# Performance work log

Hardware: AMD Instinct MI355X
Metric: run time of the kernel (lower is better)

## Reference

```python
import jax, jax.numpy as jnp
import numpy as np

LN_EPS = 1e-5

def _layernorm(x, g, b):
    mu = jnp.mean(x, axis=-1, keepdims=True)
    var = jnp.mean(jnp.square(x - mu), axis=-1, keepdims=True)
    return (x - mu) * jax.lax.rsqrt(var + LN_EPS) * g + b

def setup_inputs() -> dict:
    key = jax.random.key(0)
    ks = jax.random.split(key, 12)
    N0, N1, D0, D1, DO, E = 50000, 50000, 256, 512, 256, 1600000
    return {
        "x0": jax.random.normal(ks[0], (N0, D0), jnp.float32),
        "x1": jax.random.normal(ks[1], (N1, D1), jnp.float32),
        "W0": jax.random.normal(ks[2], (D0, DO), jnp.float32) * 0.05,
        "W1": jax.random.normal(ks[3], (D1, DO), jnp.float32) * 0.05,
        "Wres1": jax.random.normal(ks[4], (D1, DO), jnp.float32) * 0.05,
        "g0": jnp.ones((DO,), jnp.float32),
        "b0": jnp.zeros((DO,), jnp.float32),
        "g1": jnp.ones((DO,), jnp.float32),
        "b1": jnp.zeros((DO,), jnp.float32),
        "ew0": jax.random.uniform(ks[5], (E,), jnp.float32),
        "ew1": jax.random.uniform(ks[6], (E,), jnp.float32),
        "row0": jax.random.randint(ks[7], (E,), 0, N0, jnp.int32),
        "col0": jax.random.randint(ks[8], (E,), 0, N0, jnp.int32),
        "row1": jax.random.randint(ks[9], (E,), 0, N1, jnp.int32),
        "col1": jax.random.randint(ks[10], (E,), 0, N1, jnp.int32),
    }

def _gcn_type(x, W, ew, row, col, g, b, res):
    # h_proj = x @ W ; h_agg[i] = sum_{e: row_e=i} ew_e * h_proj[col_e]  (== spmm(adj, h_proj))
    h_proj = x @ W
    msgs = ew[:, None] * h_proj[col]                      # [E, DO] gather + scale
    h_agg = jax.ops.segment_sum(msgs, row, num_segments=x.shape[0])
    return _layernorm(h_agg + res, g, b)

def reference(x0, x1, W0, W1, Wres1, g0, b0, g1, b1, ew0, ew1, row0, col0, row1, col1):
    out0 = _gcn_type(x0, W0, ew0, row0, col0, g0, b0, x0)          # identity residual
    out1 = _gcn_type(x1, W1, ew1, row1, col1, g1, b1, x1 @ Wres1)  # projected residual
    return jnp.concatenate([out0, out1], axis=0)
```

## Files before the change

kernel.cpp:

```cpp
#include <hip/hip_runtime.h>
#include <hip/hip_bf16.h>
#include <cstddef>

typedef unsigned short u16;
typedef u16 u16x8 __attribute__((ext_vector_type(8)));
typedef __bf16 bf16x8 __attribute__((ext_vector_type(8)));
typedef float f32x4 __attribute__((ext_vector_type(4)));

__device__ __forceinline__ u16 f2b(float f) {
  unsigned int u = __float_as_uint(f);
  unsigned int r = 0x7FFFu + ((u >> 16) & 1u);
  return (u16)((u + r) >> 16);
}
__device__ __forceinline__ float b2f(u16 u) {
  return __uint_as_float(((unsigned int)u) << 16);
}

template <bool OUT_BF16>
__global__ __launch_bounds__(256) void gemm_bf16(
    const float* __restrict__ A, const u16* __restrict__ Bt, void* __restrict__ Cv,
    int M, int K) {
  __shared__ u16 As[128 * 64];
  __shared__ u16 Bs[128 * 64];
  const int tid = threadIdx.x;
  const int wid = tid >> 6;
  const int lane = tid & 63;
  const int brow = blockIdx.y * 128;
  const int bcol = blockIdx.x * 128;
  const int waveM = (wid >> 1) * 64;
  const int waveN = (wid & 1) * 64;
  const int q = lane >> 4;
  const int rl = lane & 15;

  f32x4 acc[4][4] = {};

  const int arow = tid >> 1;
  const int khalf = (tid & 1) * 32;
  const int garow = brow + arow;
  const bool aok = garow < M;
  const int swz = arow & 7;

  for (int k0 = 0; k0 < K; k0 += 64) {
    {
      const float* src = A + (size_t)garow * K + k0 + khalf;
      u16* dstrow = As + arow * 64;
#pragma unroll
      for (int j = 0; j < 4; ++j) {
        float4 v0 = make_float4(0.f, 0.f, 0.f, 0.f), v1 = v0;
        if (aok) {
          v0 = *(const float4*)(src + j * 8);
          v1 = *(const float4*)(src + j * 8 + 4);
        }
        u16x8 v = {f2b(v0.x), f2b(v0.y), f2b(v0.z), f2b(v0.w),
                   f2b(v1.x), f2b(v1.y), f2b(v1.z), f2b(v1.w)};
        const int c = (khalf >> 3) + j;
        *(u16x8*)(dstrow + 8 * (c ^ swz)) = v;
      }
    }
    {
      const u16* src = Bt + (size_t)(bcol + arow) * K + k0 + khalf;
      u16* dstrow = Bs + arow * 64;
#pragma unroll
      for (int j = 0; j < 4; ++j) {
        u16x8 v = *(const u16x8*)(src + j * 8);
        const int c = (khalf >> 3) + j;
        *(u16x8*)(dstrow + 8 * (c ^ swz)) = v;
      }
    }
    __syncthreads();
#pragma unroll
    for (int ks = 0; ks < 2; ++ks) {
      bf16x8 af[4], bfr[4];
      const int cbase = ks * 4 + q;
#pragma unroll
      for (int i = 0; i < 4; ++i) {
        const int r = waveM + 16 * i + rl;
        af[i] = __builtin_bit_cast(bf16x8,
                 *(const u16x8*)(As + r * 64 + 8 * (cbase ^ (rl & 7))));
      }
#pragma unroll
      for (int j = 0; j < 4; ++j) {
        const int r = waveN + 16 * j + rl;
        bfr[j] = __builtin_bit_cast(bf16x8,
                  *(const u16x8*)(Bs + r * 64 + 8 * (cbase ^ (rl & 7))));
      }
#pragma unroll
      for (int i = 0; i < 4; ++i)
#pragma unroll
        for (int j = 0; j < 4; ++j)
          acc[i][j] = __builtin_amdgcn_mfma_f32_16x16x32_bf16(af[i], bfr[j], acc[i][j], 0, 0, 0);
    }
    __syncthreads();
  }

#pragma unroll
  for (int i = 0; i < 4; ++i) {
#pragma unroll
    for (int reg = 0; reg < 4; ++reg) {
      const int gr = brow + waveM + 16 * i + q * 4 + reg;
      if (gr >= M) continue;
#pragma unroll
      for (int j = 0; j < 4; ++j) {
        const int col = bcol + waveN + 16 * j + rl;
        const float v = acc[i][j][reg];
        if (OUT_BF16) ((u16*)Cv)[(size_t)gr * 256 + col] = f2b(v);
        else          ((float*)Cv)[(size_t)gr * 256 + col] = v;
      }
    }
  }
}

__global__ __launch_bounds__(256) void conv_wt(const float* __restrict__ W,
                                               u16* __restrict__ Wt, int K) {
  const int idx = blockIdx.x * 256 + threadIdx.x;
  const int k = idx >> 8;
  const int n = idx & 255;
  if (k < K) Wt[(size_t)n * K + k] = f2b(W[idx]);
}

#define EB   256
#define RPB  128
#define NBUK 391

__global__ __launch_bounds__(256) void pa_hist(const int* __restrict__ row,
                                               int* __restrict__ ghist, int E) {
  __shared__ int h[NBUK];
  for (int i = threadIdx.x; i < NBUK; i += 256) h[i] = 0;
  __syncthreads();
  const int per = (E + EB - 1) / EB;
  const int s = blockIdx.x * per;
  const int e = min(E, s + per);
  for (int i = s + threadIdx.x; i < e; i += 256) atomicAdd(&h[row[i] >> 7], 1);
  __syncthreads();
  for (int i = threadIdx.x; i < NBUK; i += 256) ghist[i * EB + blockIdx.x] = h[i];
}

__global__ __launch_bounds__(256) void pa_scatter(
    const int* __restrict__ row, const int* __restrict__ col, const float* __restrict__ ew,
    const int* __restrict__ gscan, int2* __restrict__ tmp, int E) {
  __shared__ int cur[NBUK];
  for (int i = threadIdx.x; i < NBUK; i += 256) cur[i] = gscan[i * EB + blockIdx.x];
  __syncthreads();
  const int per = (E + EB - 1) / EB;
  const int s = blockIdx.x * per;
  const int e = min(E, s + per);
  for (int i0 = s + threadIdx.x; i0 < e; i0 += 1024) {
    int r[4], c[4], wv[4];
    bool ok[4];
#pragma unroll
    for (int j = 0; j < 4; ++j) {
      const int i = i0 + j * 256;
      ok[j] = i < e;
      if (ok[j]) { r[j] = row[i]; c[j] = col[i]; wv[j] = __float_as_int(ew[i]); }
    }
#pragma unroll
    for (int j = 0; j < 4; ++j)
      if (ok[j]) {
        const int pos = atomicAdd(&cur[r[j] >> 7], 1);
        tmp[pos] = make_int2(((r[j] & 127) << 16) | c[j], wv[j]);
      }
  }
}

__global__ __launch_bounds__(256) void pb_sort(
    const int2* __restrict__ tmp, const int* __restrict__ gscan,
    int2* __restrict__ sedge, int* __restrict__ offs, int E, int N) {
  __shared__ int h[RPB];
  __shared__ int ex[RPB];
  __shared__ int cur[RPB];
  const int b = blockIdx.x;
  const int t = threadIdx.x;
  const int base = gscan[b * EB];
  const int end = (b == NBUK - 1) ? E : gscan[(b + 1) * EB];
  if (t < RPB) h[t] = 0;
  __syncthreads();
  for (int i = base + t; i < end; i += 256) atomicAdd(&h[(tmp[i].x >> 16) & 127], 1);
  __syncthreads();
  if (t == 0) {
    int run = base;
    for (int r = 0; r < RPB; ++r) { const int cc = h[r]; ex[r] = run; cur[r] = run; run += cc; }
  }
  __syncthreads();
  if (t < RPB) {
    const int rg = b * RPB + t;
    if (rg <= N) offs[rg] = ex[t];
  }
  for (int i = base + t; i < end; i += 256) {
    const int2 v = tmp[i];
    const int pos = atomicAdd(&cur[(v.x >> 16) & 127], 1);
    sedge[pos] = make_int2(v.x & 0xFFFF, v.y);
  }
}

__global__ __launch_bounds__(256) void scan1(const int* __restrict__ deg,
                                             int* __restrict__ offs,
                                             int* __restrict__ partials, int n) {
  __shared__ int sh[256];
  const int t = threadIdx.x;
  const int base = blockIdx.x * 1024 + t * 4;
  int v[4];
#pragma unroll
  for (int j = 0; j < 4; j++) v[j] = (base + j < n) ? deg[base + j] : 0;
  const int tsum = v[0] + v[1] + v[2] + v[3];
  sh[t] = tsum;
  __syncthreads();
  for (int off = 1; off < 256; off <<= 1) {
    int x = (t >= off) ? sh[t - off] : 0;
    __syncthreads();
    sh[t] += x;
    __syncthreads();
  }
  if (t == 255) partials[blockIdx.x] = sh[255];
  int run = sh[t] - tsum;
#pragma unroll
  for (int j = 0; j < 4; j++) {
    if (base + j < n) offs[base + j] = run;
    run += v[j];
  }
}

__global__ void scan2(int* __restrict__ partials, int nb) {
  if (threadIdx.x == 0 && blockIdx.x == 0) {
    int run = 0;
    for (int i = 0; i < nb; i++) {
      int t = partials[i];
      partials[i] = run;
      run += t;
    }
  }
}

__global__ __launch_bounds__(256) void scan_add(int* __restrict__ a,
                                                const int* __restrict__ partials, int n) {
  const int t = threadIdx.x;
  const int base = blockIdx.x * 1024 + t * 4;
  const int add = partials[blockIdx.x];
#pragma unroll
  for (int j = 0; j < 4; j++)
    if (base + j < n) a[base + j] += add;
}

__global__ __launch_bounds__(256) void agg_ln(
    const u16* __restrict__ hpb, const int* __restrict__ offs,
    const int2* __restrict__ sedge,
    const float* __restrict__ res, const float* __restrict__ g, const float* __restrict__ b,
    float* __restrict__ out, int nrows) {
  const int wave = threadIdx.x >> 6;
  const int lane = threadIdx.x & 63;
  const int r = blockIdx.x * 4 + wave;
  if (r >= nrows) return;
  const int f4 = lane * 4;

  float4 acc = *(const float4*)(res + (size_t)r * 256 + f4);
  int k = offs[r];
  const int kend = offs[r + 1];
  for (; k + 3 < kend; k += 4) {
    const int2 e0 = sedge[k], e1 = sedge[k + 1], e2 = sedge[k + 2], e3 = sedge[k + 3];
    const float w0 = __int_as_float(e0.y), w1 = __int_as_float(e1.y);
    const float w2 = __int_as_float(e2.y), w3 = __int_as_float(e3.y);
    const ushort4 h0 = *(const ushort4*)(hpb + (size_t)e0.x * 256 + f4);
    const ushort4 h1 = *(const ushort4*)(hpb + (size_t)e1.x * 256 + f4);
    const ushort4 h2 = *(const ushort4*)(hpb + (size_t)e2.x * 256 + f4);
    const ushort4 h3 = *(const ushort4*)(hpb + (size_t)e3.x * 256 + f4);
    acc.x += w0 * b2f(h0.x) + w1 * b2f(h1.x) + w2 * b2f(h2.x) + w3 * b2f(h3.x);
    acc.y += w0 * b2f(h0.y) + w1 * b2f(h1.y) + w2 * b2f(h2.y) + w3 * b2f(h3.y);
    acc.z += w0 * b2f(h0.z) + w1 * b2f(h1.z) + w2 * b2f(h2.z) + w3 * b2f(h3.z);
    acc.w += w0 * b2f(h0.w) + w1 * b2f(h1.w) + w2 * b2f(h2.w) + w3 * b2f(h3.w);
  }
  for (; k < kend; ++k) {
    const int2 e = sedge[k];
    const float w = __int_as_float(e.y);
    const ushort4 h = *(const ushort4*)(hpb + (size_t)e.x * 256 + f4);
    acc.x += w * b2f(h.x); acc.y += w * b2f(h.y);
    acc.z += w * b2f(h.z); acc.w += w * b2f(h.w);
  }

  float s = acc.x + acc.y + acc.z + acc.w;
#pragma unroll
  for (int m = 32; m >= 1; m >>= 1) s += __shfl_xor(s, m);
  const float mu = s * (1.f / 256.f);
  acc.x -= mu; acc.y -= mu; acc.z -= mu; acc.w -= mu;
  float ss = acc.x * acc.x + acc.y * acc.y + acc.z * acc.z + acc.w * acc.w;
#pragma unroll
  for (int m = 32; m >= 1; m >>= 1) ss += __shfl_xor(ss, m);
  const float rs = rsqrtf(ss * (1.f / 256.f) + 1e-5f);

  const float4 gg = *(const float4*)(g + f4);
  const float4 bb = *(const float4*)(b + f4);
  float4 o;
  o.x = acc.x * rs * gg.x + bb.x;
  o.y = acc.y * rs * gg.y + bb.y;
  o.z = acc.z * rs * gg.z + bb.z;
  o.w = acc.w * rs * gg.w + bb.w;
  *(float4*)(out + (size_t)r * 256 + f4) = o;
}

extern "C" void kernel_launch(void* const* d_in, const int* in_sizes, int n_in,
                              void* d_out, int out_size, void* d_ws, size_t ws_size,
                              hipStream_t stream) {
  const float* x0    = (const float*)d_in[0];
  const float* x1    = (const float*)d_in[1];
  const float* W0    = (const float*)d_in[2];
  const float* W1    = (const float*)d_in[3];
  const float* Wres1 = (const float*)d_in[4];
  const float* g0    = (const float*)d_in[5];
  const float* b0    = (const float*)d_in[6];
  const float* g1    = (const float*)d_in[7];
  const float* b1    = (const float*)d_in[8];
  const float* ew0   = (const float*)d_in[9];
  const float* ew1   = (const float*)d_in[10];
  const int*   row0  = (const int*)d_in[11];
  const int*   col0  = (const int*)d_in[12];
  const int*   row1  = (const int*)d_in[13];
  const int*   col1  = (const int*)d_in[14];
  float* out = (float*)d_out;

  const int N = 50000, D0 = 256, D1 = 512, DO = 256, E = 1600000;

  char* w = (char*)d_ws;
  u16*   hpb   = (u16*)  (w);
  u16*   wtb   = (u16*)  (w + 25600000);
  int2*  sedge = (int2*) (w + 25862144);
  int*   offs  = (int*)  (w + 38662144);
  int*   ghist = (int*)  (w + 38862160);
  int*   parts = (int*)  (w + 39262560);
  int2*  tmp   = (int2*) (w);

  float* out0 = out;
  float* out1 = out + (size_t)N * DO;

  const dim3 blk(256);
  const dim3 gemm_grid(2, (N + 127) / 128);
  const dim3 agg_grid((N + 3) / 4);
  const int NGH = NBUK * EB;
  const int NBS = (NGH + 1023) / 1024;

  auto build_csr = [&](const int* row, const int* col, const float* ew) {
    pa_hist<<<dim3(EB), blk, 0, stream>>>(row, ghist, E);
    scan1<<<dim3(NBS), blk, 0, stream>>>(ghist, ghist, parts, NGH);
    scan2<<<dim3(1), dim3(64), 0, stream>>>(parts, NBS);
    scan_add<<<dim3(NBS), blk, 0, stream>>>(ghist, parts, NGH);
    pa_scatter<<<dim3(EB), blk, 0, stream>>>(row, col, ew, ghist, tmp, E);
    pb_sort<<<dim3(NBUK), blk, 0, stream>>>(tmp, ghist, sedge, offs, E, N);
  };

  build_csr(row0, col0, ew0);
  conv_wt<<<dim3(D0), blk, 0, stream>>>(W0, wtb, D0);
  gemm_bf16<true><<<gemm_grid, blk, 0, stream>>>(x0, wtb, hpb, N, D0);
  agg_ln<<<agg_grid, blk, 0, stream>>>(hpb, offs, sedge, x0, g0, b0, out0, N);

  conv_wt<<<dim3(D1), blk, 0, stream>>>(Wres1, wtb, D1);
  gemm_bf16<false><<<gemm_grid, blk, 0, stream>>>(x1, wtb, out1, N, D1);
  build_csr(row1, col1, ew1);
  conv_wt<<<dim3(D1), blk, 0, stream>>>(W1, wtb, D1);
  gemm_bf16<true><<<gemm_grid, blk, 0, stream>>>(x1, wtb, hpb, N, D1);
  agg_ln<<<agg_grid, blk, 0, stream>>>(hpb, offs, sedge, out1, g1, b1, out1, N);
}
```

Before: 737.6 us.

## Use full-width GEMM row tiles and split-edge 16-byte gathers in aggregation

The GEMM now uses 64x256 tiles, so each block covers all 256 output columns. Each fp32 row of A is therefore read and converted to bf16 once instead of once per column tile. In exchange the B tile in shared memory grows to 32KB. The aggregation kernel now splits each row's edges across the two half-waves. Each lane gathers 8 bf16 values with 16-byte loads, and the halves are combined with a cross-half shuffle before LayerNorm. This doubles the gather bytes per request and the independent edges in flight, at the cost of duplicated reduction work and idle lanes on the final store.

Result: faster. 707.4 us (-4.1%).

```diff
diff --git a/kernel.cpp b/kernel.cpp
--- a/kernel.cpp
+++ b/kernel.cpp
@@ -20,32 +20,32 @@
 __global__ __launch_bounds__(256) void gemm_bf16(
     const float* __restrict__ A, const u16* __restrict__ Bt, void* __restrict__ Cv,
     int M, int K) {
-  __shared__ u16 As[128 * 64];
-  __shared__ u16 Bs[128 * 64];
+  __shared__ u16 As[64 * 64];
+  __shared__ u16 Bs[256 * 64];
   const int tid = threadIdx.x;
   const int wid = tid >> 6;
   const int lane = tid & 63;
-  const int brow = blockIdx.y * 128;
-  const int bcol = blockIdx.x * 128;
-  const int waveM = (wid >> 1) * 64;
-  const int waveN = (wid & 1) * 64;
+  const int brow = blockIdx.x * 64;
+  const int waveN = wid * 64;
   const int q = lane >> 4;
   const int rl = lane & 15;
 
   f32x4 acc[4][4] = {};
 
-  const int arow = tid >> 1;
-  const int khalf = (tid & 1) * 32;
+  const int arow = tid >> 2;
+  const int kq = (tid & 3) * 16;
   const int garow = brow + arow;
   const bool aok = garow < M;
-  const int swz = arow & 7;
+  const int aswz = arow & 7;
+  const int brb = tid;
+  const int bswz = brb & 7;
 
   for (int k0 = 0; k0 < K; k0 += 64) {
     {
-      const float* src = A + (size_t)garow * K + k0 + khalf;
+      const float* src = A + (size_t)garow * K + k0 + kq;
       u16* dstrow = As + arow * 64;
 #pragma unroll
-      for (int j = 0; j < 4; ++j) {
+      for (int j = 0; j < 2; ++j) {
         float4 v0 = make_float4(0.f, 0.f, 0.f, 0.f), v1 = v0;
         if (aok) {
           v0 = *(const float4*)(src + j * 8);
@@ -53,18 +53,17 @@
         }
         u16x8 v = {f2b(v0.x), f2b(v0.y), f2b(v0.z), f2b(v0.w),
                    f2b(v1.x), f2b(v1.y), f2b(v1.z), f2b(v1.w)};
-        const int c = (khalf >> 3) + j;
-        *(u16x8*)(dstrow + 8 * (c ^ swz)) = v;
+        const int c = (kq >> 3) + j;
+        *(u16x8*)(dstrow + 8 * (c ^ aswz)) = v;
       }
     }
     {
-      const u16* src = Bt + (size_t)(bcol + arow) * K + k0 + khalf;
-      u16* dstrow = Bs + arow * 64;
-#pragma unroll
-      for (int j = 0; j < 4; ++j) {
+      const u16* src = Bt + (size_t)brb * K + k0;
+      u16* dstrow = Bs + brb * 64;
+#pragma unroll
+      for (int j = 0; j < 8; ++j) {
         u16x8 v = *(const u16x8*)(src + j * 8);
-        const int c = (khalf >> 3) + j;
-        *(u16x8*)(dstrow + 8 * (c ^ swz)) = v;
+        *(u16x8*)(dstrow + 8 * (j ^ bswz)) = v;
       }
     }
     __syncthreads();
@@ -74,7 +73,7 @@
       const int cbase = ks * 4 + q;
 #pragma unroll
       for (int i = 0; i < 4; ++i) {
-        const int r = waveM + 16 * i + rl;
+        const int r = 16 * i + rl;
         af[i] = __builtin_bit_cast(bf16x8,
                  *(const u16x8*)(As + r * 64 + 8 * (cbase ^ (rl & 7))));
       }
@@ -97,11 +96,11 @@
   for (int i = 0; i < 4; ++i) {
 #pragma unroll
     for (int reg = 0; reg < 4; ++reg) {
-      const int gr = brow + waveM + 16 * i + q * 4 + reg;
+      const int gr = brow + 16 * i + q * 4 + reg;
       if (gr >= M) continue;
 #pragma unroll
       for (int j = 0; j < 4; ++j) {
-        const int col = bcol + waveN + 16 * j + rl;
+        const int col = waveN + 16 * j + rl;
         const float v = acc[i][j][reg];
         if (OUT_BF16) ((u16*)Cv)[(size_t)gr * 256 + col] = f2b(v);
         else          ((float*)Cv)[(size_t)gr * 256 + col] = v;
@@ -249,50 +248,77 @@
   const int lane = threadIdx.x & 63;
   const int r = blockIdx.x * 4 + wave;
   if (r >= nrows) return;
-  const int f4 = lane * 4;
-
-  float4 acc = *(const float4*)(res + (size_t)r * 256 + f4);
+  const int half = lane >> 5;
+  const int f8 = (lane & 31) * 8;
+
+  float acc8[8] = {0.f, 0.f, 0.f, 0.f, 0.f, 0.f, 0.f, 0.f};
   int k = offs[r];
   const int kend = offs[r + 1];
-  for (; k + 3 < kend; k += 4) {
-    const int2 e0 = sedge[k], e1 = sedge[k + 1], e2 = sedge[k + 2], e3 = sedge[k + 3];
-    const float w0 = __int_as_float(e0.y), w1 = __int_as_float(e1.y);
-    const float w2 = __int_as_float(e2.y), w3 = __int_as_float(e3.y);
-    const ushort4 h0 = *(const ushort4*)(hpb + (size_t)e0.x * 256 + f4);
-    const ushort4 h1 = *(const ushort4*)(hpb + (size_t)e1.x * 256 + f4);
-    const ushort4 h2 = *(const ushort4*)(hpb + (size_t)e2.x * 256 + f4);
-    const ushort4 h3 = *(const ushort4*)(hpb + (size_t)e3.x * 256 + f4);
-    acc.x += w0 * b2f(h0.x) + w1 * b2f(h1.x) + w2 * b2f(h2.x) + w3 * b2f(h3.x);
-    acc.y += w0 * b2f(h0.y) + w1 * b2f(h1.y) + w2 * b2f(h2.y) + w3 * b2f(h3.y);
-    acc.z += w0 * b2f(h0.z) + w1 * b2f(h1.z) + w2 * b2f(h2.z) + w3 * b2f(h3.z);
-    acc.w += w0 * b2f(h0.w) + w1 * b2f(h1.w) + w2 * b2f(h2.w) + w3 * b2f(h3.w);
-  }
-  for (; k < kend; ++k) {
-    const int2 e = sedge[k];
+  for (; k + 7 < kend; k += 8) {
+    int2 e[4];
+#pragma unroll
+    for (int j = 0; j < 4; ++j) e[j] = sedge[k + half + 2 * j];
+    u16x8 h[4];
+#pragma unroll
+    for (int j = 0; j < 4; ++j)
+      h[j] = *(const u16x8*)(hpb + (size_t)e[j].x * 256 + f8);
+#pragma unroll
+    for (int j = 0; j < 4; ++j) {
+      const float w = __int_as_float(e[j].y);
+#pragma unroll
+      for (int d = 0; d < 8; ++d) acc8[d] += w * b2f(h[j][d]);
+    }
+  }
+  for (int kc = k + half; kc < kend; kc += 2) {
+    const int2 e = sedge[kc];
     const float w = __int_as_float(e.y);
-    const ushort4 h = *(const ushort4*)(hpb + (size_t)e.x * 256 + f4);
-    acc.x += w * b2f(h.x); acc.y += w * b2f(h.y);
-    acc.z += w * b2f(h.z); acc.w += w * b2f(h.w);
-  }
-
-  float s = acc.x + acc.y + acc.z + acc.w;
+    const u16x8 h = *(const u16x8*)(hpb + (size_t)e.x * 256 + f8);
+#pragma unroll
+    for (int d = 0; d < 8; ++d) acc8[d] += w * b2f(h[d]);
+  }
+
+#pragma unroll
+  for (int d = 0; d < 8; ++d) acc8[d] += __shfl_xor(acc8[d], 32);
+
+  {
+    const float4 r0 = *(const float4*)(res + (size_t)r * 256 + f8);
+    const float4 r1 = *(const float4*)(res + (size_t)r * 256 + f8 + 4);
+    acc8[0] += r0.x; acc8[1] += r0.y; acc8[2] += r0.z; acc8[3] += r0.w;
+    acc8[4] += r1.x; acc8[5] += r1.y; acc8[6] += r1.z; acc8[7] += r1.w;
+  }
+
+  float s = 0.f;
+#pragma unroll
+  for (int d = 0; d < 8; ++d) s += acc8[d];
 #pragma unroll
   for (int m = 32; m >= 1; m >>= 1) s += __shfl_xor(s, m);
-  const float mu = s * (1.f / 256.f);
-  acc.x -= mu; acc.y -= mu; acc.z -= mu; acc.w -= mu;
-  float ss = acc.x * acc.x + acc.y * acc.y + acc.z * acc.z + acc.w * acc.w;
+  const float mu = s * (1.f / 512.f);
+#pragma unroll
+  for (int d = 0; d < 8; ++d) acc8[d] -= mu;
+  float ss = 0.f;
+#pragma unroll
+  for (int d = 0; d < 8; ++d) ss += acc8[d] * acc8[d];
 #pragma unroll
   for (int m = 32; m >= 1; m >>= 1) ss += __shfl_xor(ss, m);
-  const float rs = rsqrtf(ss * (1.f / 256.f) + 1e-5f);
-
-  const float4 gg = *(const float4*)(g + f4);
-  const float4 bb = *(const float4*)(b + f4);
-  float4 o;
-  o.x = acc.x * rs * gg.x + bb.x;
-  o.y = acc.y * rs * gg.y + bb.y;
-  o.z = acc.z * rs * gg.z + bb.z;
-  o.w = acc.w * rs * gg.w + bb.w;
-  *(float4*)(out + (size_t)r * 256 + f4) = o;
+  const float rs = rsqrtf(ss * (1.f / 512.f) + 1e-5f);
+
+  if (half == 0) {
+    const float4 g0v = *(const float4*)(g + f8);
+    const float4 g1v = *(const float4*)(g + f8 + 4);
+    const float4 b0v = *(const float4*)(b + f8);
+    const float4 b1v = *(const float4*)(b + f8 + 4);
+    float4 o0, o1;
+    o0.x = acc8[0] * rs * g0v.x + b0v.x;
+    o0.y = acc8[1] * rs * g0v.y + b0v.y;
+    o0.z = acc8[2] * rs * g0v.z + b0v.z;
+    o0.w = acc8[3] * rs * g0v.w + b0v.w;
+    o1.x = acc8[4] * rs * g1v.x + b1v.x;
+    o1.y = acc8[5] * rs * g1v.y + b1v.y;
+    o1.z = acc8[6] * rs * g1v.z + b1v.z;
+    o1.w = acc8[7] * rs * g1v.w + b1v.w;
+    *(float4*)(out + (size_t)r * 256 + f8) = o0;
+    *(float4*)(out + (size_t)r * 256 + f8 + 4) = o1;
+  }
 }
 
 extern "C" void kernel_launch(void* const* d_in, const int* in_sizes, int n_in,
@@ -330,7 +356,7 @@
   float* out1 = out + (size_t)N * DO;
 
   const dim3 blk(256);
-  const dim3 gemm_grid(2, (N + 127) / 128);
+  const dim3 gemm_grid((N + 63) / 64);
   const dim3 agg_grid((N + 3) / 4);
   const int NGH = NBUK * EB;
   const int NBS = (NGH + 1023) / 1024;
```
